# Kernel tuning notes

Hardware: AMD Instinct MI355X
Metric: run time of the kernel (lower is better)

The kernel has to match this reference:

```python
import jax, jax.numpy as jnp
import numpy as np

B, S, IN, E, H, NH = 32, 1024, 16, 128, 256, 4
DH = E // NH
EPS = 1e-5


def _ln(x, g, b):
    mu = jnp.mean(x, axis=-1, keepdims=True)
    var = jnp.mean(jnp.square(x - mu), axis=-1, keepdims=True)
    return (x - mu) * jax.lax.rsqrt(var + EPS) * g + b


def setup_inputs() -> dict:
    key = jax.random.key(0)
    ks = iter(jax.random.split(key, 32))
    n = lambda shape, s=0.02: jax.random.normal(next(ks), shape, jnp.float32) * s
    inp = {
        "x": jax.random.normal(next(ks), (B, S, IN), jnp.float32),
        "mask": jax.random.uniform(next(ks), (B, S), jnp.float32),
        "embed_w": n((E, IN)), "embed_b": jnp.zeros((E,), jnp.float32),
        # 3 encoder layers, params stacked on leading layer axis
        "in_proj_w": n((3, 3 * E, E)), "in_proj_b": jnp.zeros((3, 3 * E), jnp.float32),
        "out_w": n((3, E, E)), "out_b": jnp.zeros((3, E), jnp.float32),
        "ln1_g": jnp.ones((3, E), jnp.float32), "ln1_b": jnp.zeros((3, E), jnp.float32),
        "ln2_g": jnp.ones((3, E), jnp.float32), "ln2_b": jnp.zeros((3, E), jnp.float32),
        "ffn_w1": n((3, E, E)), "ffn_b1": jnp.zeros((3, E), jnp.float32),
        "ffn_w2": n((3, E, E)), "ffn_b2": jnp.zeros((3, E), jnp.float32),
        "cls_w1": n((H, E)), "cls_b1": jnp.zeros((H,), jnp.float32),
        "cls_w2": n((H, H)), "cls_b2": jnp.zeros((H,), jnp.float32),
        "cls_w3": n((H, H)), "cls_b3": jnp.zeros((H,), jnp.float32),
        "cls_w4": n((1, H)), "cls_b4": jnp.zeros((1,), jnp.float32),
    }
    return inp


def _encoder_layer(x, ipw, ipb, ow, ob, g1, b1, g2, b2, w1, fb1, w2, fb2):
    # PyTorch TransformerEncoderLayer, norm_first=False (post-norm), relu FFN
    qkv = x @ ipw.T + ipb                      # [B,S,3E]
    q, k, v = jnp.split(qkv, 3, axis=-1)
    q = q.reshape(B, S, NH, DH).transpose(0, 2, 1, 3)
    k = k.reshape(B, S, NH, DH).transpose(0, 2, 1, 3)
    v = v.reshape(B, S, NH, DH).transpose(0, 2, 1, 3)
    scores = jnp.einsum("bhqd,bhkd->bhqk", q, k) / np.sqrt(DH)  # naive O(S^2) math SDPA
    attn = jax.nn.softmax(scores, axis=-1)
    o = jnp.einsum("bhqk,bhkd->bhqd", attn, v)
    o = o.transpose(0, 2, 1, 3).reshape(B, S, E) @ ow.T + ob
    x = _ln(x + o, g1, b1)
    ff = jax.nn.relu(x @ w1.T + fb1) @ w2.T + fb2
    return _ln(x + ff, g2, b2)


def reference(x, mask, embed_w, embed_b, in_proj_w, in_proj_b, out_w, out_b,
              ln1_g, ln1_b, ln2_g, ln2_b, ffn_w1, ffn_b1, ffn_w2, ffn_b2,
              cls_w1, cls_b1, cls_w2, cls_b2, cls_w3, cls_b3, cls_w4, cls_b4):
    h = jax.nn.relu(x @ embed_w.T + embed_b)   # [B,S,E]
    for i in range(3):
        h = _encoder_layer(h, in_proj_w[i], in_proj_b[i], out_w[i], out_b[i],
                           ln1_g[i], ln1_b[i], ln2_g[i], ln2_b[i],
                           ffn_w1[i], ffn_b1[i], ffn_w2[i], ffn_b2[i])
    pooled = jnp.sum(h * mask[:, :, None], axis=1)  # [B,E] masked sum pool
    z = jax.nn.relu(pooled @ cls_w1.T + cls_b1)
    z = jax.nn.relu(z @ cls_w2.T + cls_b2)
    z = jax.nn.relu(z @ cls_w3.T + cls_b3)
    return jax.nn.sigmoid(z @ cls_w4.T + cls_b4)    # [B,1]
```

## Files before the change

### kernel.cpp

```cpp
#include <hip/hip_runtime.h>
#include <hip/hip_bf16.h>
#include <math.h>

#define B 32
#define S 1024
#define IN_DIM 16
#define E 128
#define NH 4
#define DH 32
#define HDIM 256
#define ROWS (B*S)
#define EPS 1e-5f

#define N_IPW (3*384*128)
#define N_SQ  (3*128*128)
#define NCVT ((N_IPW + 3*N_SQ) / 256)

typedef __bf16 bf16x8 __attribute__((ext_vector_type(8)));
typedef __bf16 bf16x4 __attribute__((ext_vector_type(4)));
typedef __bf16 bf16x2 __attribute__((ext_vector_type(2)));
typedef float f32x4 __attribute__((ext_vector_type(4)));

union BF2U { bf16x2 b; unsigned int u; };
__device__ inline unsigned int pk2(float a, float b) {
    BF2U x; x.b[0] = (__bf16)a; x.b[1] = (__bf16)b; return x.u;
}

union U8 { bf16x8 v8; bf16x4 v4[2]; };
__device__ inline void st8(__bf16* p, bf16x8 v) {
    U8 u; u.v8 = v;
    *(bf16x4*)p = u.v4[0];
    *(bf16x4*)(p + 4) = u.v4[1];
}
__device__ inline bf16x8 ld8(const __bf16* p) {
    U8 u;
    u.v4[0] = *(const bf16x4*)p;
    u.v4[1] = *(const bf16x4*)(p + 4);
    return u.v8;
}

__global__ __launch_bounds__(256) void k_embedcvt(
        const float* __restrict__ ipw, const float* __restrict__ ow,
        const float* __restrict__ w1, const float* __restrict__ w2,
        __bf16* __restrict__ wbo,
        const float* __restrict__ x, const float* __restrict__ W,
        const float* __restrict__ bias, __bf16* __restrict__ hb)
{
    int t = threadIdx.x;
    if (blockIdx.x < NCVT) {
        int i = blockIdx.x * 256 + t;
        float v;
        if (i < N_IPW) v = ipw[i];
        else if (i < N_IPW + N_SQ) v = ow[i - N_IPW];
        else if (i < N_IPW + 2 * N_SQ) v = w1[i - N_IPW - N_SQ];
        else v = w2[i - N_IPW - 2 * N_SQ];
        wbo[i] = (__bf16)v;
        return;
    }
    int row0 = (blockIdx.x - NCVT) * 16;
    __shared__ float xs[16][16];
    xs[t >> 4][t & 15] = x[(row0 + (t >> 4)) * IN_DIM + (t & 15)];
    __syncthreads();
    int sub = t >> 7, tc = t & 127;
    float w[16];
#pragma unroll
    for (int i = 0; i < 16; ++i) w[i] = W[tc * 16 + i];
    float bb = bias[tc];
#pragma unroll
    for (int rr = 0; rr < 8; ++rr) {
        int lr = sub * 8 + rr;
        float acc = bb;
#pragma unroll
        for (int i = 0; i < 16; ++i) acc += xs[lr][i] * w[i];
        hb[(size_t)(row0 + lr) * E + tc] = (__bf16)fmaxf(acc, 0.f);
    }
}

__global__ __launch_bounds__(256) void k_gemm_qkv(const __bf16* __restrict__ A,
        const __bf16* __restrict__ W, const float* __restrict__ bias,
        __bf16* __restrict__ qk, __bf16* __restrict__ vt)
{
    __shared__ __attribute__((aligned(16))) __bf16 As[128][132];
    __shared__ __attribute__((aligned(16))) __bf16 Ws[64][132];
    int t = threadIdx.x;
    int m0 = blockIdx.y * 128, n0 = blockIdx.x * 64;
    {
        int arow = t >> 1, acol = (t & 1) * 64;
        const __bf16* Ap = A + (size_t)(m0 + arow) * 128 + acol;
#pragma unroll
        for (int j = 0; j < 8; ++j)
            st8(&As[arow][acol + j * 8], *(const bf16x8*)&Ap[j * 8]);
        int wrow = t >> 2, wcol = (t & 3) * 32;
        const __bf16* Wp = W + (size_t)(n0 + wrow) * 128 + wcol;
#pragma unroll
        for (int j = 0; j < 4; ++j)
            st8(&Ws[wrow][wcol + j * 8], *(const bf16x8*)&Wp[j * 8]);
    }
    __syncthreads();
    int lane = t & 63, wv = t >> 6;
    int l15 = lane & 15, quad = lane >> 4;
    int wm = (wv & 1) * 64, wn = (wv >> 1) * 32;
    f32x4 acc[2][4];
#pragma unroll
    for (int i = 0; i < 2; ++i)
#pragma unroll
        for (int j = 0; j < 4; ++j) acc[i][j] = (f32x4){0.f, 0.f, 0.f, 0.f};
#pragma unroll
    for (int kc = 0; kc < 4; ++kc) {
        bf16x8 aw[2], ba[4];
#pragma unroll
        for (int nc = 0; nc < 2; ++nc)
            aw[nc] = ld8(&Ws[wn + nc * 16 + l15][kc * 32 + quad * 8]);
#pragma unroll
        for (int mc = 0; mc < 4; ++mc)
            ba[mc] = ld8(&As[wm + mc * 16 + l15][kc * 32 + quad * 8]);
#pragma unroll
        for (int nc = 0; nc < 2; ++nc)
#pragma unroll
            for (int mc = 0; mc < 4; ++mc)
                acc[nc][mc] = __builtin_amdgcn_mfma_f32_16x16x32_bf16(aw[nc], ba[mc], acc[nc][mc], 0, 0, 0);
    }
#pragma unroll
    for (int nc = 0; nc < 2; ++nc) {
        float4 bv = *(const float4*)&bias[n0 + wn + nc * 16 + quad * 4];
#pragma unroll
        for (int mc = 0; mc < 4; ++mc) {
            float v0 = acc[nc][mc][0] + bv.x;
            float v1 = acc[nc][mc][1] + bv.y;
            float v2 = acc[nc][mc][2] + bv.z;
            float v3 = acc[nc][mc][3] + bv.w;
            int n = n0 + wn + nc * 16 + quad * 4;
            int m = m0 + wm + mc * 16 + l15;
            if (n < 256) {
                uint2 u; u.x = pk2(v0, v1); u.y = pk2(v2, v3);
                *(uint2*)&qk[(size_t)m * 256 + n] = u;
            } else {
                int dp = n - 256;
                int hq = dp >> 5, d0 = dp & 31;
                __bf16* vp = vt + (((size_t)(m >> 10) * 4 + hq) * 32 + d0) * 1024 + (m & 1023);
                vp[0] = (__bf16)v0; vp[1024] = (__bf16)v1;
                vp[2048] = (__bf16)v2; vp[3072] = (__bf16)v3;
            }
        }
    }
}

__global__ __launch_bounds__(256) void k_attn3(const __bf16* __restrict__ qk,
        const __bf16* __restrict__ vt, __bf16* __restrict__ O)
{
    int qt = blockIdx.x & 7, bh = blockIdx.x >> 3;
    int hh = bh & 3, b = bh >> 2;
    __shared__ __attribute__((aligned(16))) __bf16 Kb[2][64][36];
    __shared__ __attribute__((aligned(16))) __bf16 Vb[2][32][68];
    __shared__ __attribute__((aligned(16))) __bf16 Pm[4][16][68];
    int t = threadIdx.x, lane = t & 63, wv = t >> 6;
    int l15 = lane & 15, quad = lane >> 4;
    const __bf16* qbase = qk + (size_t)(b * S) * 256 + hh * 32;
    const __bf16* kbase = qk + (size_t)(b * S) * 256 + 128 + hh * 32;
    const __bf16* vbase = vt + ((size_t)(b * 4 + hh) * 32) * 1024;
    const float qscale = 0.1767766952966369f * 1.4426950408889634f;

    bf16x8 bQ[2];
#pragma unroll
    for (int gq = 0; gq < 2; ++gq) {
        bf16x8 qv = *(const bf16x8*)&qbase[(size_t)(qt * 128 + gq * 64 + wv * 16 + l15) * 256 + quad * 8];
#pragma unroll
        for (int j = 0; j < 8; ++j) bQ[gq][j] = (__bf16)((float)qv[j] * qscale);
    }

    int ksr = t >> 2, ksc = (t & 3) * 8;
    int vsr = t >> 3, vsc = (t & 7) * 8;

    {
        bf16x8 k0 = *(const bf16x8*)&kbase[(size_t)ksr * 256 + ksc];
        bf16x8 v0 = *(const bf16x8*)&vbase[(size_t)vsr * 1024 + vsc];
        st8(&Kb[0][ksr][ksc], k0);
        st8(&Vb[0][vsr][vsc], v0);
    }
    __syncthreads();

    float l_acc[2] = {0.f, 0.f};
    f32x4 o[2][2];
#pragma unroll
    for (int gq = 0; gq < 2; ++gq)
#pragma unroll
        for (int j = 0; j < 2; ++j) o[gq][j] = (f32x4){0.f, 0.f, 0.f, 0.f};

    for (int it = 0; it < 16; ++it) {
        const int cur = it & 1;
        bf16x8 knext, vnext;
        if (it < 15) {
            knext = *(const bf16x8*)&kbase[(size_t)((it + 1) * 64 + ksr) * 256 + ksc];
            vnext = *(const bf16x8*)&vbase[(size_t)vsr * 1024 + (it + 1) * 64 + vsc];
        }
        bf16x8 aK[4];
#pragma unroll
        for (int c = 0; c < 4; ++c)
            aK[c] = ld8(&Kb[cur][c * 16 + l15][quad * 8]);
        bf16x8 bv[2][2];
#pragma unroll
        for (int kc = 0; kc < 2; ++kc) {
            bv[kc][0] = ld8(&Vb[cur][l15][kc * 32 + quad * 8]);
            bv[kc][1] = ld8(&Vb[cur][16 + l15][kc * 32 + quad * 8]);
        }
#pragma unroll
        for (int gq = 0; gq < 2; ++gq) {
            f32x4 sf[4];
#pragma unroll
            for (int c = 0; c < 4; ++c)
                sf[c] = __builtin_amdgcn_mfma_f32_16x16x32_bf16(aK[c], bQ[gq], (f32x4){0.f, 0.f, 0.f, 0.f}, 0, 0, 0);
#pragma unroll
            for (int c = 0; c < 4; ++c) {
                float p0 = __builtin_amdgcn_exp2f(sf[c][0]);
                float p1 = __builtin_amdgcn_exp2f(sf[c][1]);
                float p2 = __builtin_amdgcn_exp2f(sf[c][2]);
                float p3 = __builtin_amdgcn_exp2f(sf[c][3]);
                l_acc[gq] += (p0 + p1) + (p2 + p3);
                uint2 u; u.x = pk2(p0, p1); u.y = pk2(p2, p3);
                *(uint2*)&Pm[wv][l15][c * 16 + quad * 4] = u;
            }
            __asm__ __volatile__("" ::: "memory");
#pragma unroll
            for (int kc = 0; kc < 2; ++kc) {
                bf16x8 ap = ld8(&Pm[wv][l15][kc * 32 + quad * 8]);
                o[gq][0] = __builtin_amdgcn_mfma_f32_16x16x32_bf16(ap, bv[kc][0], o[gq][0], 0, 0, 0);
                o[gq][1] = __builtin_amdgcn_mfma_f32_16x16x32_bf16(ap, bv[kc][1], o[gq][1], 0, 0, 0);
            }
            __asm__ __volatile__("" ::: "memory");
        }
        if (it < 15) {
            st8(&Kb[cur ^ 1][ksr][ksc], knext);
            st8(&Vb[cur ^ 1][vsr][vsc], vnext);
            __syncthreads();
        }
    }

#pragma unroll
    for (int gq = 0; gq < 2; ++gq) {
        float la = l_acc[gq];
        la += __shfl_xor(la, 16);
        la += __shfl_xor(la, 32);
#pragma unroll
        for (int reg = 0; reg < 4; ++reg) {
            int qloc = quad * 4 + reg;
            float linv = 1.f / __shfl(la, qloc);
            int row = qt * 128 + gq * 64 + wv * 16 + qloc;
            __bf16* op = O + ((size_t)(b * S) + row) * E + hh * 32;
            op[l15] = (__bf16)(o[gq][0][reg] * linv);
            op[16 + l15] = (__bf16)(o[gq][1][reg] * linv);
        }
    }
}

__global__ __launch_bounds__(256) void k_layer2(const __bf16* __restrict__ t0b,
        const __bf16* __restrict__ Wo, const float* __restrict__ ob,
        const float* __restrict__ g1, const float* __restrict__ bt1,
        const __bf16* __restrict__ W1, const float* __restrict__ b1v,
        const __bf16* __restrict__ W2, const float* __restrict__ b2v,
        const float* __restrict__ g2, const float* __restrict__ bt2,
        __bf16* __restrict__ hb)
{
    __shared__ __attribute__((aligned(16))) __bf16 As[64][132];
    __shared__ __attribute__((aligned(16))) __bf16 Ws[128][132];
    __shared__ float red[2][64][2];
    int t = threadIdx.x;
    int m0 = blockIdx.x * 64;
    int arow = t >> 2, acol = (t & 3) * 32;
    int wrow = t >> 1, wcol = (t & 1) * 64;
    {
        const __bf16* Ap = t0b + (size_t)(m0 + arow) * 128 + acol;
#pragma unroll
        for (int j = 0; j < 4; ++j)
            st8(&As[arow][acol + j * 8], *(const bf16x8*)&Ap[j * 8]);
        const __bf16* Wp = Wo + (size_t)wrow * 128 + wcol;
#pragma unroll
        for (int j = 0; j < 8; ++j)
            st8(&Ws[wrow][wcol + j * 8], *(const bf16x8*)&Wp[j * 8]);
    }
    __syncthreads();
    int lane = t & 63, wv = t >> 6;
    int l15 = lane & 15, quad = lane >> 4;
    int nh = wv & 1, mh = wv >> 1;
    f32x4 acc[4][2];

#pragma unroll
    for (int i = 0; i < 4; ++i)
#pragma unroll
        for (int j = 0; j < 2; ++j) acc[i][j] = (f32x4){0.f, 0.f, 0.f, 0.f};
#pragma unroll
    for (int kc = 0; kc < 4; ++kc) {
        bf16x8 aw[4], ba[2];
#pragma unroll
        for (int nc = 0; nc < 4; ++nc)
            aw[nc] = ld8(&Ws[nh * 64 + nc * 16 + l15][kc * 32 + quad * 8]);
#pragma unroll
        for (int mc = 0; mc < 2; ++mc)
            ba[mc] = ld8(&As[mh * 32 + mc * 16 + l15][kc * 32 + quad * 8]);
#pragma unroll
        for (int nc = 0; nc < 4; ++nc)
#pragma unroll
            for (int mc = 0; mc < 2; ++mc)
                acc[nc][mc] = __builtin_amdgcn_mfma_f32_16x16x32_bf16(aw[nc], ba[mc], acc[nc][mc], 0, 0, 0);
    }
    float s1[2] = {0.f, 0.f}, s2[2] = {0.f, 0.f};
#pragma unroll
    for (int nc = 0; nc < 4; ++nc) {
        float4 bv = *(const float4*)&ob[nh * 64 + nc * 16 + quad * 4];
#pragma unroll
        for (int mc = 0; mc < 2; ++mc) {
            int m = m0 + mh * 32 + mc * 16 + l15;
            bf16x4 rv = *(const bf16x4*)&hb[(size_t)m * 128 + nh * 64 + nc * 16 + quad * 4];
            acc[nc][mc][0] += bv.x + (float)rv[0];
            acc[nc][mc][1] += bv.y + (float)rv[1];
            acc[nc][mc][2] += bv.z + (float)rv[2];
            acc[nc][mc][3] += bv.w + (float)rv[3];
#pragma unroll
            for (int i = 0; i < 4; ++i) {
                s1[mc] += acc[nc][mc][i];
                s2[mc] += acc[nc][mc][i] * acc[nc][mc][i];
            }
        }
    }
#pragma unroll
    for (int mc = 0; mc < 2; ++mc) {
        s1[mc] += __shfl_xor(s1[mc], 16); s1[mc] += __shfl_xor(s1[mc], 32);
        s2[mc] += __shfl_xor(s2[mc], 16); s2[mc] += __shfl_xor(s2[mc], 32);
    }
    if (quad == 0) {
#pragma unroll
        for (int mc = 0; mc < 2; ++mc) {
            red[nh][mh * 32 + mc * 16 + l15][0] = s1[mc];
            red[nh][mh * 32 + mc * 16 + l15][1] = s2[mc];
        }
    }
    __syncthreads();
    float mu[2], rs[2];
#pragma unroll
    for (int mc = 0; mc < 2; ++mc) {
        int r = mh * 32 + mc * 16 + l15;
        float S1 = red[0][r][0] + red[1][r][0];
        float S2 = red[0][r][1] + red[1][r][1];
        mu[mc] = S1 * (1.f / 128.f);
        float var = S2 * (1.f / 128.f) - mu[mc] * mu[mc];
        rs[mc] = rsqrtf(var + EPS);
    }
    bf16x4 res2[4][2];
#pragma unroll
    for (int nc = 0; nc < 4; ++nc) {
        float4 gv = *(const float4*)&g1[nh * 64 + nc * 16 + quad * 4];
        float4 bb = *(const float4*)&bt1[nh * 64 + nc * 16 + quad * 4];
#pragma unroll
        for (int mc = 0; mc < 2; ++mc) {
            float o0 = (acc[nc][mc][0] - mu[mc]) * rs[mc] * gv.x + bb.x;
            float o1 = (acc[nc][mc][1] - mu[mc]) * rs[mc] * gv.y + bb.y;
            float o2 = (acc[nc][mc][2] - mu[mc]) * rs[mc] * gv.z + bb.z;
            float o3 = (acc[nc][mc][3] - mu[mc]) * rs[mc] * gv.w + bb.w;
            bf16x4 xb;
            xb[0] = (__bf16)o0; xb[1] = (__bf16)o1;
            xb[2] = (__bf16)o2; xb[3] = (__bf16)o3;
            res2[nc][mc] = xb;
            *(bf16x4*)&As[mh * 32 + mc * 16 + l15][nh * 64 + nc * 16 + quad * 4] = xb;
        }
    }
    {
        const __bf16* Wp = W1 + (size_t)wrow * 128 + wcol;
#pragma unroll
        for (int j = 0; j < 8; ++j)
            st8(&Ws[wrow][wcol + j * 8], *(const bf16x8*)&Wp[j * 8]);
    }
    __syncthreads();

#pragma unroll
    for (int i = 0; i < 4; ++i)
#pragma unroll
        for (int j = 0; j < 2; ++j) acc[i][j] = (f32x4){0.f, 0.f, 0.f, 0.f};
#pragma unroll
    for (int kc = 0; kc < 4; ++kc) {
        bf16x8 aw[4], ba[2];
#pragma unroll
        for (int nc = 0; nc < 4; ++nc)
            aw[nc] = ld8(&Ws[nh * 64 + nc * 16 + l15][kc * 32 + quad * 8]);
#pragma unroll
        for (int mc = 0; mc < 2; ++mc)
            ba[mc] = ld8(&As[mh * 32 + mc * 16 + l15][kc * 32 + quad * 8]);
#pragma unroll
        for (int nc = 0; nc < 4; ++nc)
#pragma unroll
            for (int mc = 0; mc < 2; ++mc)
                acc[nc][mc] = __builtin_amdgcn_mfma_f32_16x16x32_bf16(aw[nc], ba[mc], acc[nc][mc], 0, 0, 0);
    }
    __syncthreads();
#pragma unroll
    for (int nc = 0; nc < 4; ++nc) {
        float4 bv = *(const float4*)&b1v[nh * 64 + nc * 16 + quad * 4];
#pragma unroll
        for (int mc = 0; mc < 2; ++mc) {
            float v0 = fmaxf(acc[nc][mc][0] + bv.x, 0.f);
            float v1 = fmaxf(acc[nc][mc][1] + bv.y, 0.f);
            float v2 = fmaxf(acc[nc][mc][2] + bv.z, 0.f);
            float v3 = fmaxf(acc[nc][mc][3] + bv.w, 0.f);
            uint2 u; u.x = pk2(v0, v1); u.y = pk2(v2, v3);
            *(uint2*)&As[mh * 32 + mc * 16 + l15][nh * 64 + nc * 16 + quad * 4] = u;
        }
    }
    {
        const __bf16* Wp = W2 + (size_t)wrow * 128 + wcol;
#pragma unroll
        for (int j = 0; j < 8; ++j)
            st8(&Ws[wrow][wcol + j * 8], *(const bf16x8*)&Wp[j * 8]);
    }
    __syncthreads();

#pragma unroll
    for (int i = 0; i < 4; ++i)
#pragma unroll
        for (int j = 0; j < 2; ++j) acc[i][j] = (f32x4){0.f, 0.f, 0.f, 0.f};
#pragma unroll
    for (int kc = 0; kc < 4; ++kc) {
        bf16x8 aw[4], ba[2];
#pragma unroll
        for (int nc = 0; nc < 4; ++nc)
            aw[nc] = ld8(&Ws[nh * 64 + nc * 16 + l15][kc * 32 + quad * 8]);
#pragma unroll
        for (int mc = 0; mc < 2; ++mc)
            ba[mc] = ld8(&As[mh * 32 + mc * 16 + l15][kc * 32 + quad * 8]);
#pragma unroll
        for (int nc = 0; nc < 4; ++nc)
#pragma unroll
            for (int mc = 0; mc < 2; ++mc)
                acc[nc][mc] = __builtin_amdgcn_mfma_f32_16x16x32_bf16(aw[nc], ba[mc], acc[nc][mc], 0, 0, 0);
    }
    s1[0] = s1[1] = s2[0] = s2[1] = 0.f;
#pragma unroll
    for (int nc = 0; nc < 4; ++nc) {
        float4 bv = *(const float4*)&b2v[nh * 64 + nc * 16 + quad * 4];
#pragma unroll
        for (int mc = 0; mc < 2; ++mc) {
            acc[nc][mc][0] += bv.x + (float)res2[nc][mc][0];
            acc[nc][mc][1] += bv.y + (float)res2[nc][mc][1];
            acc[nc][mc][2] += bv.z + (float)res2[nc][mc][2];
            acc[nc][mc][3] += bv.w + (float)res2[nc][mc][3];
#pragma unroll
            for (int i = 0; i < 4; ++i) {
                s1[mc] += acc[nc][mc][i];
                s2[mc] += acc[nc][mc][i] * acc[nc][mc][i];
            }
        }
    }
#pragma unroll
    for (int mc = 0; mc < 2; ++mc) {
        s1[mc] += __shfl_xor(s1[mc], 16); s1[mc] += __shfl_xor(s1[mc], 32);
        s2[mc] += __shfl_xor(s2[mc], 16); s2[mc] += __shfl_xor(s2[mc], 32);
    }
    if (quad == 0) {
#pragma unroll
        for (int mc = 0; mc < 2; ++mc) {
            red[nh][mh * 32 + mc * 16 + l15][0] = s1[mc];
            red[nh][mh * 32 + mc * 16 + l15][1] = s2[mc];
        }
    }
    __syncthreads();
#pragma unroll
    for (int mc = 0; mc < 2; ++mc) {
        int r = mh * 32 + mc * 16 + l15;
        float S1 = red[0][r][0] + red[1][r][0];
        float S2 = red[0][r][1] + red[1][r][1];
        mu[mc] = S1 * (1.f / 128.f);
        float var = S2 * (1.f / 128.f) - mu[mc] * mu[mc];
        rs[mc] = rsqrtf(var + EPS);
    }
#pragma unroll
    for (int nc = 0; nc < 4; ++nc) {
        float4 gv = *(const float4*)&g2[nh * 64 + nc * 16 + quad * 4];
        float4 bb = *(const float4*)&bt2[nh * 64 + nc * 16 + quad * 4];
#pragma unroll
        for (int mc = 0; mc < 2; ++mc) {
            int m = m0 + mh * 32 + mc * 16 + l15;
            float o0 = (acc[nc][mc][0] - mu[mc]) * rs[mc] * gv.x + bb.x;
            float o1 = (acc[nc][mc][1] - mu[mc]) * rs[mc] * gv.y + bb.y;
            float o2 = (acc[nc][mc][2] - mu[mc]) * rs[mc] * gv.z + bb.z;
            float o3 = (acc[nc][mc][3] - mu[mc]) * rs[mc] * gv.w + bb.w;
            uint2 u; u.x = pk2(o0, o1); u.y = pk2(o2, o3);
            *(uint2*)&hb[(size_t)m * 128 + nh * 64 + nc * 16 + quad * 4] = u;
        }
    }
}

__global__ __launch_bounds__(128) void k_pool1(const __bf16* __restrict__ h,
        const float* __restrict__ mask, float* __restrict__ part)
{
    int bx = blockIdx.x;
    int b = bx >> 3, ch = bx & 7, t = threadIdx.x;
    float acc = 0.f;
    const __bf16* hp = h + (size_t)(b * S + ch * 128) * E + t;
    const float* mp = mask + b * S + ch * 128;
    for (int s = 0; s < 128; ++s) acc += (float)hp[(size_t)s * E] * mp[s];
    part[(size_t)bx * E + t] = acc;
}

__global__ __launch_bounds__(256) void k_head(const float* __restrict__ part,
        const float* __restrict__ cw1, const float* __restrict__ cb1,
        const float* __restrict__ cw2, const float* __restrict__ cb2,
        const float* __restrict__ cw3, const float* __restrict__ cb3,
        const float* __restrict__ cw4, const float* __restrict__ cb4,
        float* __restrict__ out)
{
    int b = blockIdx.x, t = threadIdx.x;
    __shared__ float p[128], za[256], zb[256];
    __shared__ float red4[4];
    if (t < 128) {
        float a = 0.f;
#pragma unroll
        for (int c = 0; c < 8; ++c) a += part[(size_t)(b * 8 + c) * 128 + t];
        p[t] = a;
    }
    __syncthreads();
    float a1 = cb1[t];
    for (int k = 0; k < 128; ++k) a1 += p[k] * cw1[t * 128 + k];
    za[t] = fmaxf(a1, 0.f);
    __syncthreads();
    float a2 = cb2[t];
    for (int k = 0; k < 256; ++k) a2 += za[k] * cw2[t * 256 + k];
    zb[t] = fmaxf(a2, 0.f);
    __syncthreads();
    float a3 = cb3[t];
    for (int k = 0; k < 256; ++k) a3 += zb[k] * cw3[t * 256 + k];
    float z3 = fmaxf(a3, 0.f);
    float prt = z3 * cw4[t];
#pragma unroll
    for (int o2 = 32; o2; o2 >>= 1) prt += __shfl_xor(prt, o2);
    if ((t & 63) == 0) red4[t >> 6] = prt;
    __syncthreads();
    if (t == 0) {
        float sum = red4[0] + red4[1] + red4[2] + red4[3] + cb4[0];
        out[b] = 1.f / (1.f + __expf(-sum));
    }
}

extern "C" void kernel_launch(void* const* d_in, const int* in_sizes, int n_in,
                              void* d_out, int out_size, void* d_ws, size_t ws_size,
                              hipStream_t stream)
{
    const float* x     = (const float*)d_in[0];
    const float* mask  = (const float*)d_in[1];
    const float* emb_w = (const float*)d_in[2];
    const float* emb_b = (const float*)d_in[3];
    const float* ipw   = (const float*)d_in[4];
    const float* ipb   = (const float*)d_in[5];
    const float* ow    = (const float*)d_in[6];
    const float* ob    = (const float*)d_in[7];
    const float* ln1g  = (const float*)d_in[8];
    const float* ln1b  = (const float*)d_in[9];
    const float* ln2g  = (const float*)d_in[10];
    const float* ln2b  = (const float*)d_in[11];
    const float* w1    = (const float*)d_in[12];
    const float* fb1   = (const float*)d_in[13];
    const float* w2    = (const float*)d_in[14];
    const float* fb2   = (const float*)d_in[15];
    const float* cw1   = (const float*)d_in[16];
    const float* cb1   = (const float*)d_in[17];
    const float* cw2   = (const float*)d_in[18];
    const float* cb2   = (const float*)d_in[19];
    const float* cw3   = (const float*)d_in[20];
    const float* cb3   = (const float*)d_in[21];
    const float* cw4   = (const float*)d_in[22];
    const float* cb4   = (const float*)d_in[23];

    char* p = (char*)d_ws;
    __bf16* hb   = (__bf16*)p;   p += (size_t)ROWS * E * 2;
    __bf16* qkb  = (__bf16*)p;   p += (size_t)ROWS * 256 * 2;
    __bf16* vtb  = (__bf16*)p;   p += (size_t)ROWS * 32 * 4 * 2 / 4;
    __bf16* t0b  = (__bf16*)p;   p += (size_t)ROWS * E * 2;
    __bf16* wb   = (__bf16*)p;   p += (size_t)(N_IPW + 3 * N_SQ) * 2;
    float* part  = (float*)p;    p += (size_t)B * 8 * E * 4;

    __bf16* wb_ipw = wb;
    __bf16* wb_ow  = wb + N_IPW;
    __bf16* wb_w1  = wb_ow + N_SQ;
    __bf16* wb_w2  = wb_w1 + N_SQ;

    k_embedcvt<<<NCVT + ROWS / 16, 256, 0, stream>>>(
        ipw, ow, w1, w2, wb, x, emb_w, emb_b, hb);
    for (int L = 0; L < 3; ++L) {
        k_gemm_qkv<<<dim3(6, ROWS / 128), 256, 0, stream>>>(
            hb, wb_ipw + (size_t)L * 384 * 128, ipb + L * 384, qkb, vtb);
        k_attn3<<<B * NH * (S / 128), 256, 0, stream>>>(qkb, vtb, t0b);
        k_layer2<<<ROWS / 64, 256, 0, stream>>>(
            t0b, wb_ow + (size_t)L * 128 * 128, ob + L * 128,
            ln1g + L * E, ln1b + L * E,
            wb_w1 + (size_t)L * 128 * 128, fb1 + L * 128,
            wb_w2 + (size_t)L * 128 * 128, fb2 + L * 128,
            ln2g + L * E, ln2b + L * E, hb);
    }
    k_pool1<<<B * 8, 128, 0, stream>>>(hb, mask, part);
    k_head<<<B, 256, 0, stream>>>(part, cw1, cb1, cw2, cb2, cw3, cb3, cw4, cb4,
                                  (float*)d_out);
}
```

Before: 336.1 us.

## Replace exp2 with Schraudolph bit-trick exp and compute row sums via MFMA

The attention kernel drops the hardware exp2 and instead computes exp approximately with the Schraudolph trick. Q is prescaled by 2^23, the bias constant is folded into the MFMA accumulator init, and the score is converted to an integer whose high 16 bits are taken as the bf16 probability. The softmax denominator now comes from an extra MFMA against a vector of ones, which removes the scalar adds and cross-lane shuffles. The P staging buffer is doubled so both query groups are written before the PV MFMAs run. This cuts VALU work per score, but the piecewise-linear exp approximation lowers accuracy and there is no max subtraction, so large scores could overflow.

```diff
diff --git a/kernel.cpp b/kernel.cpp
--- a/kernel.cpp
+++ b/kernel.cpp
@@ -145,20 +145,25 @@
     }
 }
 
-__global__ __launch_bounds__(256) void k_attn3(const __bf16* __restrict__ qk,
+__global__ __launch_bounds__(256) void k_attn4(const __bf16* __restrict__ qk,
         const __bf16* __restrict__ vt, __bf16* __restrict__ O)
 {
     int qt = blockIdx.x & 7, bh = blockIdx.x >> 3;
     int hh = bh & 3, b = bh >> 2;
     __shared__ __attribute__((aligned(16))) __bf16 Kb[2][64][36];
     __shared__ __attribute__((aligned(16))) __bf16 Vb[2][32][68];
-    __shared__ __attribute__((aligned(16))) __bf16 Pm[4][16][68];
+    __shared__ __attribute__((aligned(16))) __bf16 Pm[2][4][16][68];
     int t = threadIdx.x, lane = t & 63, wv = t >> 6;
     int l15 = lane & 15, quad = lane >> 4;
     const __bf16* qbase = qk + (size_t)(b * S) * 256 + hh * 32;
     const __bf16* kbase = qk + (size_t)(b * S) * 256 + 128 + hh * 32;
     const __bf16* vbase = vt + ((size_t)(b * 4 + hh) * 32) * 1024;
-    const float qscale = 0.1767766952966369f * 1.4426950408889634f;
+    const float qscale = 0.1767766952966369f * 1.4426950408889634f * 8388608.0f;
+    const float C2 = 1065101558.0f;
+    const f32x4 cinit = {C2, C2, C2, C2};
+    bf16x8 vones;
+#pragma unroll
+    for (int j = 0; j < 8; ++j) vones[j] = (__bf16)1.0f;
 
     bf16x8 bQ[2];
 #pragma unroll
@@ -179,12 +184,13 @@
     }
     __syncthreads();
 
-    float l_acc[2] = {0.f, 0.f};
-    f32x4 o[2][2];
-#pragma unroll
-    for (int gq = 0; gq < 2; ++gq)
+    f32x4 o[2][2], ol[2];
+#pragma unroll
+    for (int gq = 0; gq < 2; ++gq) {
+        ol[gq] = (f32x4){0.f, 0.f, 0.f, 0.f};
 #pragma unroll
         for (int j = 0; j < 2; ++j) o[gq][j] = (f32x4){0.f, 0.f, 0.f, 0.f};
+    }
 
     for (int it = 0; it < 16; ++it) {
         const int cur = it & 1;
@@ -208,26 +214,31 @@
             f32x4 sf[4];
 #pragma unroll
             for (int c = 0; c < 4; ++c)
-                sf[c] = __builtin_amdgcn_mfma_f32_16x16x32_bf16(aK[c], bQ[gq], (f32x4){0.f, 0.f, 0.f, 0.f}, 0, 0, 0);
+                sf[c] = __builtin_amdgcn_mfma_f32_16x16x32_bf16(aK[c], bQ[gq], cinit, 0, 0, 0);
 #pragma unroll
             for (int c = 0; c < 4; ++c) {
-                float p0 = __builtin_amdgcn_exp2f(sf[c][0]);
-                float p1 = __builtin_amdgcn_exp2f(sf[c][1]);
-                float p2 = __builtin_amdgcn_exp2f(sf[c][2]);
-                float p3 = __builtin_amdgcn_exp2f(sf[c][3]);
-                l_acc[gq] += (p0 + p1) + (p2 + p3);
-                uint2 u; u.x = pk2(p0, p1); u.y = pk2(p2, p3);
-                *(uint2*)&Pm[wv][l15][c * 16 + quad * 4] = u;
+                int i0 = (int)sf[c][0];
+                int i1 = (int)sf[c][1];
+                int i2 = (int)sf[c][2];
+                int i3 = (int)sf[c][3];
+                uint2 u;
+                u.x = __builtin_amdgcn_perm((unsigned)i1, (unsigned)i0, 0x07060302u);
+                u.y = __builtin_amdgcn_perm((unsigned)i3, (unsigned)i2, 0x07060302u);
+                *(uint2*)&Pm[gq][wv][l15][c * 16 + quad * 4] = u;
             }
-            __asm__ __volatile__("" ::: "memory");
+        }
+        __asm__ __volatile__("" ::: "memory");
+#pragma unroll
+        for (int gq = 0; gq < 2; ++gq) {
 #pragma unroll
             for (int kc = 0; kc < 2; ++kc) {
-                bf16x8 ap = ld8(&Pm[wv][l15][kc * 32 + quad * 8]);
+                bf16x8 ap = ld8(&Pm[gq][wv][l15][kc * 32 + quad * 8]);
                 o[gq][0] = __builtin_amdgcn_mfma_f32_16x16x32_bf16(ap, bv[kc][0], o[gq][0], 0, 0, 0);
                 o[gq][1] = __builtin_amdgcn_mfma_f32_16x16x32_bf16(ap, bv[kc][1], o[gq][1], 0, 0, 0);
+                ol[gq]   = __builtin_amdgcn_mfma_f32_16x16x32_bf16(ap, vones, ol[gq], 0, 0, 0);
             }
-            __asm__ __volatile__("" ::: "memory");
-        }
+        }
+        __asm__ __volatile__("" ::: "memory");
         if (it < 15) {
             st8(&Kb[cur ^ 1][ksr][ksc], knext);
             st8(&Vb[cur ^ 1][vsr][vsc], vnext);
@@ -237,14 +248,10 @@
 
 #pragma unroll
     for (int gq = 0; gq < 2; ++gq) {
-        float la = l_acc[gq];
-        la += __shfl_xor(la, 16);
-        la += __shfl_xor(la, 32);
 #pragma unroll
         for (int reg = 0; reg < 4; ++reg) {
-            int qloc = quad * 4 + reg;
-            float linv = 1.f / __shfl(la, qloc);
-            int row = qt * 128 + gq * 64 + wv * 16 + qloc;
+            float linv = 1.f / ol[gq][reg];
+            int row = qt * 128 + gq * 64 + wv * 16 + quad * 4 + reg;
             __bf16* op = O + ((size_t)(b * S) + row) * E + hh * 32;
             op[l15] = (__bf16)(o[gq][0][reg] * linv);
             op[16 + l15] = (__bf16)(o[gq][1][reg] * linv);
@@ -584,7 +591,7 @@
     for (int L = 0; L < 3; ++L) {
         k_gemm_qkv<<<dim3(6, ROWS / 128), 256, 0, stream>>>(
             hb, wb_ipw + (size_t)L * 384 * 128, ipb + L * 384, qkb, vtb);
-        k_attn3<<<B * NH * (S / 128), 256, 0, stream>>>(qkb, vtb, t0b);
+        k_attn4<<<B * NH * (S / 128), 256, 0, stream>>>(qkb, vtb, t0b);
         k_layer2<<<ROWS / 64, 256, 0, stream>>>(
             t0b, wb_ow + (size_t)L * 128 * 128, ob + L * 128,
             ln1g + L * E, ln1b + L * E,
```

New measurement: 328.3 us. 1.02x faster.
